# Optimization experiments

Hardware: AMD Instinct MI355X
Metric: run time of the kernel (lower is better)

Reference implementation:

```python
import jax, jax.numpy as jnp
import numpy as np

# QLSTMClassifier (quantum mode): Embedding -> QLSTM (4 quantum gate layers per step) -> Linear -> log_softmax.
# NOTE: QLSTM.forward unbinds dim 0 (batch) and cats each x:(seq,emb) with hx:(batch,hid),
# which requires batch == seq_len. We honor that with S = batch = seq_len.
S = 256   # batch == seq_len
E = 1024  # embedding_dim
H = 10    # hidden_dim == n_qubits (required by f*cx elementwise product)
V = 50257 # vocab_size
T = 50    # tagset_size


def setup_inputs() -> dict:
    key = jax.random.key(0)
    ks = jax.random.split(key, 6)
    sentence = jax.random.randint(ks[0], (S, S), 0, V)                                   # (batch, seq)
    emb_table = jax.random.normal(ks[1], (V, E), jnp.float32) * 0.02                      # nn.Embedding weight
    Wg = jax.random.normal(ks[2], (4, E + H, H), jnp.float32) * (1.0 / np.sqrt(E + H))    # forget/input/update/output linears
    bg = jnp.zeros((4, H), jnp.float32)
    theta = jax.random.normal(ks[3], (4, H), jnp.float32)                                 # trainable RX angles per gate
    W_out = jax.random.normal(ks[4], (H, T), jnp.float32) * (1.0 / np.sqrt(H))            # hidden2tag
    b_out = jnp.zeros((T,), jnp.float32)
    return dict(sentence=sentence, emb_table=emb_table, Wg=Wg, bg=bg,
                theta=theta, W_out=W_out, b_out=b_out)


def _qlayer(z, th):
    # Exact closed form of the QLayer circuit on n wires starting from |0...0>:
    #   RX(z_w) then RX(th_w) on wire w  ==> RX(a_w) with a_w = z_w + th_w (product state),
    #   then CNOT ring: CNOT(0,1), CNOT(1,2), ..., CNOT(n-2,n-1), CNOT(n-1,0),
    # Heisenberg-picture pullback of Z_w through the CNOT ring gives
    #   M_0 = Z_1 Z_2 ... Z_{n-1},   M_w = Z_0 Z_1 ... Z_w  (w >= 1),
    # and on the product state <Z_j> = cos(a_j), so expectations factorize:
    #   out_0 = prod_{j>=1} cos(a_j),  out_w = prod_{j<=w} cos(a_j).
    c = jnp.cos(z + th)                                   # (B, H)
    cum = jnp.cumprod(c, axis=-1)                         # prefix products
    tail = jnp.prod(c[:, 1:], axis=-1, keepdims=True)     # wire-0 observable
    return jnp.concatenate([tail, cum[:, 1:]], axis=-1)   # (B, H)


def reference(sentence, emb_table, Wg, bg, theta, W_out, b_out):
    embeds = emb_table[sentence]                          # (S, S, E); scan axis = dim 0 (unbind dim)
    h0 = jnp.zeros((embeds.shape[0], theta.shape[1]), embeds.dtype)

    def step(carry, x):                                   # x: (S, E)
        hx, cx = carry
        comb = jnp.concatenate([x, hx], axis=-1)          # (S, E+H)
        z = jnp.einsum('bi,gio->gbo', comb, Wg) + bg[:, None, :]  # (4, S, H)
        f = jax.nn.sigmoid(_qlayer(z[0], theta[0]))
        i = jax.nn.sigmoid(_qlayer(z[1], theta[1]))
        g = jnp.tanh(_qlayer(z[2], theta[2]))
        o = jax.nn.sigmoid(_qlayer(z[3], theta[3]))
        cx = f * cx + i * g
        hx = o * jnp.tanh(cx)
        return (hx, cx), hx

    _, outs = jax.lax.scan(step, (h0, h0), embeds)        # (S, S, H)
    logits = outs @ W_out + b_out                         # (S, S, T)
    return jax.nn.log_softmax(logits, axis=2)
```

## Files before the change

### kernel.cpp

```cpp
#include <hip/hip_runtime.h>
#include <hip/hip_bf16.h>


#define E_DIM 1024
#define H_DIM 10
#define NC 40
#define EHS 10340

typedef __attribute__((ext_vector_type(8))) short bf16x8;
typedef __attribute__((ext_vector_type(4))) float f32x4;

__device__ __forceinline__ unsigned short f2bf(float f) {
    unsigned u = __float_as_uint(f);
    unsigned r = u + 0x7FFFu + ((u >> 16) & 1u);
    return (unsigned short)(r >> 16);
}

__global__ __launch_bounds__(256) void k_wt(const float* __restrict__ Wg,
                                            unsigned short* __restrict__ Bfg) {
    int i = blockIdx.x * 256 + threadIdx.x;
    if (i >= 6144) return;
    int lane = i & 63, nt = (i >> 6) % 3, c = i / 192;
    int kg = lane >> 4, n = lane & 15;
    int nc = nt * 16 + n;
    unsigned short v[8];
#pragma unroll
    for (int j = 0; j < 8; ++j) {
        int k = c * 32 + kg * 8 + j;
        float w = 0.0f;
        if (nc < NC) {
            int g = nc / H_DIM, h = nc % H_DIM;
            w = Wg[g * EHS + k * H_DIM + h];
        }
        v[j] = f2bf(w);
    }
    bf16x8* dst = (bf16x8*)(Bfg + (size_t)i * 8);
    bf16x8 pk;
#pragma unroll
    for (int j = 0; j < 8; ++j) pk[j] = (short)v[j];
    *dst = pk;
}

__global__ __launch_bounds__(256, 4) void k_gemm(const int* __restrict__ idx,
                                                 const float* __restrict__ emb,
                                                 const unsigned short* __restrict__ Bfg,
                                                 float* __restrict__ zs) {
    const int tid = threadIdx.x;
    const int wave = tid >> 6, lane = tid & 63;
    const int R0 = (blockIdx.x * 4 + wave) * 16;
    const int m = lane & 15, q = lane >> 4;

    const int token = idx[R0 + m];
    const float* arow = emb + (size_t)token * E_DIM + q * 8;

    f32x4 acc0 = {0.f, 0.f, 0.f, 0.f}, acc1 = acc0, acc2 = acc0;

#pragma unroll 2
    for (int c = 0; c < 32; ++c) {
        float4 a0 = *(const float4*)(arow + c * 32);
        float4 a1 = *(const float4*)(arow + c * 32 + 4);
        bf16x8 b0 = *(const bf16x8*)(Bfg + ((size_t)(c * 3 + 0) * 64 + lane) * 8);
        bf16x8 b1 = *(const bf16x8*)(Bfg + ((size_t)(c * 3 + 1) * 64 + lane) * 8);
        bf16x8 b2 = *(const bf16x8*)(Bfg + ((size_t)(c * 3 + 2) * 64 + lane) * 8);
        bf16x8 af;
        af[0] = (short)f2bf(a0.x); af[1] = (short)f2bf(a0.y);
        af[2] = (short)f2bf(a0.z); af[3] = (short)f2bf(a0.w);
        af[4] = (short)f2bf(a1.x); af[5] = (short)f2bf(a1.y);
        af[6] = (short)f2bf(a1.z); af[7] = (short)f2bf(a1.w);
        acc0 = __builtin_amdgcn_mfma_f32_16x16x32_bf16(af, b0, acc0, 0, 0, 0);
        acc1 = __builtin_amdgcn_mfma_f32_16x16x32_bf16(af, b1, acc1, 0, 0, 0);
        acc2 = __builtin_amdgcn_mfma_f32_16x16x32_bf16(af, b2, acc2, 0, 0, 0);
    }

    const int t = R0 >> 8;
    const int bbase = (R0 & 255) + q * 4;
#pragma unroll
    for (int i = 0; i < 4; ++i) {
        int b = bbase + i;
        size_t o = ((size_t)b * 256 + t) * NC;
        zs[o + m] = acc0[i];
        zs[o + 16 + m] = acc1[i];
        if (m < 8) zs[o + 32 + m] = acc2[i];
    }
}

template <int CTRL>
__device__ __forceinline__ float dpp1(float x) {
    return __int_as_float(__builtin_amdgcn_update_dpp(
        __float_as_int(1.0f), __float_as_int(x), CTRL, 0xF, 0xF, false));
}
#define ROW_SHR(n) (0x110 + (n))
#define ROW_SHL(n) (0x100 + (n))

__device__ __forceinline__ float rdlane(float v, int l) {
    return __int_as_float(__builtin_amdgcn_readlane(__float_as_int(v), l));
}

__global__ __launch_bounds__(128) void k_rnn(const float* __restrict__ zs,
                                             const float* __restrict__ Wg,
                                             const float* __restrict__ bg,
                                             const float* __restrict__ theta,
                                             float* __restrict__ outs) {
    __shared__ float zbuf[2][640];
    const int tid = threadIdx.x;
    const int b = blockIdx.x;

    if (tid >= 64) {
        const int p = tid - 64;
        const float* src = zs + (size_t)b * 256 * NC;
#pragma unroll
        for (int k = 0; k < 10; ++k) zbuf[0][p + k * 64] = src[p + k * 64];
        __syncthreads();
        for (int blk = 0; blk < 16; ++blk) {
            if (blk + 1 < 16) {
                const float* s2 = src + (blk + 1) * 640;
                float v[10];
#pragma unroll
                for (int k = 0; k < 10; ++k) v[k] = s2[p + k * 64];
#pragma unroll
                for (int k = 0; k < 10; ++k) zbuf[(blk + 1) & 1][p + k * 64] = v[k];
            }
            __syncthreads();
        }
    } else {
        const int lane = tid;
        const int r = lane >> 4;
        const int h = lane & 15;
        const int hc = (h < 10) ? h : 9;
        const int cidx = r * 10 + hc;

        float Wh[10];
#pragma unroll
        for (int j = 0; j < 10; ++j) Wh[j] = Wg[r * EHS + (E_DIM + j) * H_DIM + hc];
        const float bias = bg[cidx] + theta[cidx];

        const float kk = (r == 2) ? 2.0f : -1.0f;
        const float aa = (r == 2) ? 1.0f : 0.0f;
        const float bb = (r == 2) ? -2.0f : 1.0f;

        float cx = 0.0f, hx = 0.0f;
        __syncthreads();

        for (int blk = 0; blk < 16; ++blk) {
            const float* zb = zbuf[blk & 1];
            float zv = zb[cidx];
#pragma unroll 4
            for (int s = 0; s < 16; ++s) {
                float znext = zb[((s < 15) ? (s + 1) * 40 : s * 40) + cidx];

                float hv0 = rdlane(hx, 0), hv1 = rdlane(hx, 1), hv2 = rdlane(hx, 2),
                      hv3 = rdlane(hx, 3), hv4 = rdlane(hx, 4), hv5 = rdlane(hx, 5),
                      hv6 = rdlane(hx, 6), hv7 = rdlane(hx, 7), hv8 = rdlane(hx, 8),
                      hv9 = rdlane(hx, 9);
                float d0 = fmaf(hv0, Wh[0], fmaf(hv2, Wh[2],
                           fmaf(hv4, Wh[4], fmaf(hv6, Wh[6], hv8 * Wh[8]))));
                float d1 = fmaf(hv1, Wh[1], fmaf(hv3, Wh[3],
                           fmaf(hv5, Wh[5], fmaf(hv7, Wh[7], hv9 * Wh[9]))));
                float z = (zv + bias) + (d0 + d1);

                float cc = __builtin_amdgcn_cosf(z * 0.15915494309189535f);

                float pp = cc;
                pp *= dpp1<ROW_SHR(1)>(pp);
                pp *= dpp1<ROW_SHR(2)>(pp);
                pp *= dpp1<ROW_SHR(4)>(pp);
                pp *= dpp1<ROW_SHR(8)>(pp);
                float ss = (h < 10) ? cc : 1.0f;
                ss *= dpp1<ROW_SHL(1)>(ss);
                ss *= dpp1<ROW_SHL(2)>(ss);
                ss *= dpp1<ROW_SHL(4)>(ss);
                ss *= dpp1<ROW_SHL(8)>(ss);
                float tl = dpp1<ROW_SHL(1)>(ss);
                float qv = (h == 0) ? tl : pp;

                float e = __expf(kk * qv);
                float act = fmaf(bb, __builtin_amdgcn_rcpf(1.0f + e), aa);

                float fv = __shfl(act, h);
                float iv = __shfl(act, 16 + h);
                float gv = __shfl(act, 32 + h);
                float ov = __shfl(act, 48 + h);

                cx = fmaf(fv, cx, iv * gv);
                float e2 = __expf(2.0f * cx);
                float th = fmaf(-2.0f, __builtin_amdgcn_rcpf(1.0f + e2), 1.0f);
                hx = ov * th;

                int t = blk * 16 + s;
                if (lane < 10) outs[((size_t)t * 256 + b) * H_DIM + lane] = hx;
                zv = znext;
            }
            __syncthreads();
        }
    }
}

__global__ __launch_bounds__(256) void k_head(const float* __restrict__ outs,
                                              const float* __restrict__ Wo,
                                              const float* __restrict__ bo,
                                              float* __restrict__ out) {
    const size_t row = blockIdx.x * 256 + threadIdx.x;
    float hx[10];
#pragma unroll
    for (int i = 0; i < 5; ++i) {
        float2 v = *(const float2*)&outs[row * H_DIM + 2 * i];
        hx[2 * i] = v.x; hx[2 * i + 1] = v.y;
    }
    float lg[50];
#pragma unroll
    for (int cI = 0; cI < 50; ++cI) {
        float l = bo[cI];
#pragma unroll
        for (int j = 0; j < 10; ++j) l = fmaf(hx[j], Wo[j * 50 + cI], l);
        lg[cI] = l;
    }
    float m = lg[0];
#pragma unroll
    for (int cI = 1; cI < 50; ++cI) m = fmaxf(m, lg[cI]);
    float sum = 0.0f;
#pragma unroll
    for (int cI = 0; cI < 50; ++cI) sum += __expf(lg[cI] - m);
    float lse = m + __logf(sum);
#pragma unroll
    for (int i = 0; i < 25; ++i) {
        float2 v = {lg[2 * i] - lse, lg[2 * i + 1] - lse};
        *(float2*)&out[row * 50 + 2 * i] = v;
    }
}

extern "C" void kernel_launch(void* const* d_in, const int* in_sizes, int n_in,
                              void* d_out, int out_size, void* d_ws, size_t ws_size,
                              hipStream_t stream) {
    const int*   sentence = (const int*)d_in[0];
    const float* emb      = (const float*)d_in[1];
    const float* Wg       = (const float*)d_in[2];
    const float* bg       = (const float*)d_in[3];
    const float* theta    = (const float*)d_in[4];
    const float* Wo       = (const float*)d_in[5];
    const float* bo       = (const float*)d_in[6];
    float* out = (float*)d_out;

    float* ws = (float*)d_ws;
    unsigned short* Bfg = (unsigned short*)ws;
    float* zs   = ws + 24576;
    float* outs = zs + (size_t)256 * 256 * NC;

    k_wt<<<24, 256, 0, stream>>>(Wg, Bfg);
    k_gemm<<<1024, 256, 0, stream>>>(sentence, emb, Bfg, zs);
    k_rnn<<<256, 128, 0, stream>>>(zs, Wg, bg, theta, outs);
    k_head<<<256, 256, 0, stream>>>(outs, Wo, bo, out);
}
```

Before: 382.6 us.

## Stage embedding rows through LDS with coalesced row-wide loads in GEMM

The gather GEMM now has each wave load whole embedding rows with contiguous float4 loads across all 64 lanes, 256 columns at a time. It converts them to bf16 and stores them in a padded per-wave LDS tile, then reads the MFMA A fragments from LDS. Before, each lane fetched 32-byte pieces at strided offsets from 16 different rows, so accesses were poorly coalesced. The change adds LDS traffic, 16 float4 registers per lane in flight, and roughly 33 KB of shared memory per block, which may reduce occupancy. No barrier is used because each wave only touches its own tile.

```diff
diff --git a/kernel.cpp b/kernel.cpp
--- a/kernel.cpp
+++ b/kernel.cpp
@@ -6,6 +6,7 @@
 #define H_DIM 10
 #define NC 40
 #define EHS 10340
+#define ALD 264
 
 typedef __attribute__((ext_vector_type(8))) short bf16x8;
 typedef __attribute__((ext_vector_type(4))) float f32x4;
@@ -23,7 +24,7 @@
     int lane = i & 63, nt = (i >> 6) % 3, c = i / 192;
     int kg = lane >> 4, n = lane & 15;
     int nc = nt * 16 + n;
-    unsigned short v[8];
+    bf16x8 pk;
 #pragma unroll
     for (int j = 0; j < 8; ++j) {
         int k = c * 32 + kg * 8 + j;
@@ -32,44 +33,51 @@
             int g = nc / H_DIM, h = nc % H_DIM;
             w = Wg[g * EHS + k * H_DIM + h];
         }
-        v[j] = f2bf(w);
-    }
-    bf16x8* dst = (bf16x8*)(Bfg + (size_t)i * 8);
-    bf16x8 pk;
-#pragma unroll
-    for (int j = 0; j < 8; ++j) pk[j] = (short)v[j];
-    *dst = pk;
+        pk[j] = (short)f2bf(w);
+    }
+    *(bf16x8*)(Bfg + (size_t)i * 8) = pk;
 }
 
 __global__ __launch_bounds__(256, 4) void k_gemm(const int* __restrict__ idx,
                                                  const float* __restrict__ emb,
                                                  const unsigned short* __restrict__ Bfg,
                                                  float* __restrict__ zs) {
+    __shared__ unsigned short As[4][16 * ALD];
     const int tid = threadIdx.x;
     const int wave = tid >> 6, lane = tid & 63;
     const int R0 = (blockIdx.x * 4 + wave) * 16;
     const int m = lane & 15, q = lane >> 4;
-
-    const int token = idx[R0 + m];
-    const float* arow = emb + (size_t)token * E_DIM + q * 8;
+    unsigned short* myA = &As[wave][0];
+
+    int tok[16];
+#pragma unroll
+    for (int r = 0; r < 16; ++r) tok[r] = idx[R0 + r];
 
     f32x4 acc0 = {0.f, 0.f, 0.f, 0.f}, acc1 = acc0, acc2 = acc0;
 
-#pragma unroll 2
-    for (int c = 0; c < 32; ++c) {
-        float4 a0 = *(const float4*)(arow + c * 32);
-        float4 a1 = *(const float4*)(arow + c * 32 + 4);
-        bf16x8 b0 = *(const bf16x8*)(Bfg + ((size_t)(c * 3 + 0) * 64 + lane) * 8);
-        bf16x8 b1 = *(const bf16x8*)(Bfg + ((size_t)(c * 3 + 1) * 64 + lane) * 8);
-        bf16x8 b2 = *(const bf16x8*)(Bfg + ((size_t)(c * 3 + 2) * 64 + lane) * 8);
-        bf16x8 af;
-        af[0] = (short)f2bf(a0.x); af[1] = (short)f2bf(a0.y);
-        af[2] = (short)f2bf(a0.z); af[3] = (short)f2bf(a0.w);
-        af[4] = (short)f2bf(a1.x); af[5] = (short)f2bf(a1.y);
-        af[6] = (short)f2bf(a1.z); af[7] = (short)f2bf(a1.w);
-        acc0 = __builtin_amdgcn_mfma_f32_16x16x32_bf16(af, b0, acc0, 0, 0, 0);
-        acc1 = __builtin_amdgcn_mfma_f32_16x16x32_bf16(af, b1, acc1, 0, 0, 0);
-        acc2 = __builtin_amdgcn_mfma_f32_16x16x32_bf16(af, b2, acc2, 0, 0, 0);
+    for (int kq = 0; kq < 4; ++kq) {
+        float4 rv[16];
+#pragma unroll
+        for (int r = 0; r < 16; ++r)
+            rv[r] = *(const float4*)(emb + (size_t)tok[r] * E_DIM + kq * 256 + lane * 4);
+#pragma unroll
+        for (int r = 0; r < 16; ++r) {
+            unsigned lo = ((unsigned)f2bf(rv[r].y) << 16) | f2bf(rv[r].x);
+            unsigned hi = ((unsigned)f2bf(rv[r].w) << 16) | f2bf(rv[r].z);
+            uint2 pk = {lo, hi};
+            *(uint2*)(myA + r * ALD + lane * 4) = pk;
+        }
+#pragma unroll
+        for (int cc = 0; cc < 8; ++cc) {
+            const int c = kq * 8 + cc;
+            bf16x8 af = *(const bf16x8*)(myA + m * ALD + cc * 32 + q * 8);
+            bf16x8 b0 = *(const bf16x8*)(Bfg + ((size_t)(c * 3 + 0) * 64 + lane) * 8);
+            bf16x8 b1 = *(const bf16x8*)(Bfg + ((size_t)(c * 3 + 1) * 64 + lane) * 8);
+            bf16x8 b2 = *(const bf16x8*)(Bfg + ((size_t)(c * 3 + 2) * 64 + lane) * 8);
+            acc0 = __builtin_amdgcn_mfma_f32_16x16x32_bf16(af, b0, acc0, 0, 0, 0);
+            acc1 = __builtin_amdgcn_mfma_f32_16x16x32_bf16(af, b1, acc1, 0, 0, 0);
+            acc2 = __builtin_amdgcn_mfma_f32_16x16x32_bf16(af, b2, acc2, 0, 0, 0);
+        }
     }
 
     const int t = R0 >> 8;
```

After: 384.3 us. No clear change (+0.5%).
